# Performance work log

Measured on AMD Instinct MI355X. Metric: run time of the kernel, lower is better.

Reference implementation:

```python
import jax, jax.numpy as jnp
import numpy as np

N_EDGES = 8_388_608      # total synapses (flat weight vector length)
NUM_TYPES = 200          # number of unique edge types (ragged groups)
STRENGTH = 1e-3          # regularizer strength (cast to float32 as in the TF module)


def setup_inputs() -> dict:
    key = jax.random.key(0)
    k1, k2, k3 = jax.random.split(key, 3)
    # Edges pre-sorted by edge type -> contiguous segments (equivalent to the
    # RaggedTensor.from_value_rowids grouping built in __init__).
    segment_ids = jnp.sort(
        jax.random.randint(k1, (N_EDGES,), 0, NUM_TYPES, dtype=jnp.int32))
    x = jax.random.normal(k2, (N_EDGES,), dtype=jnp.float32)
    init_raw = jax.random.normal(k3, (N_EDGES,), dtype=jnp.float32)
    # __init__ sorts the initial weights within each edge-type group; since
    # segment_ids is already sorted, lexsort with segment_ids as the primary
    # key sorts values within each contiguous segment.
    order = jnp.lexsort((init_raw, segment_ids))
    initial_sorted = init_raw[order]
    return {"x": x, "initial_sorted": initial_sorted, "segment_ids": segment_ids}


def reference(x, initial_sorted, segment_ids):
    x = x.astype(jnp.float32)
    # Segmented sort of the current weights: primary key = edge type,
    # secondary key = value. Equivalent to tf.sort(x_i) per ragged group.
    order = jnp.lexsort((x, segment_ids))
    x_sorted = x[order]                       # [n_edges], sorted within each group
    diff = jnp.abs(x_sorted - initial_sorted)  # per-edge |sorted(x) - sorted(y)|
    sums = jax.ops.segment_sum(diff, segment_ids, num_segments=NUM_TYPES)
    counts = jax.ops.segment_sum(jnp.ones_like(diff), segment_ids,
                                 num_segments=NUM_TYPES)
    emd = sums / jnp.maximum(counts, 1.0)      # per-group Wasserstein-1 (mean L1)
    return jnp.mean(emd) * jnp.float32(STRENGTH)
```

## Files before the change

### kernel.cpp

```cpp
#include <hip/hip_runtime.h>
#include <hip/hip_bf16.h>

#define NSEG 200
#define STRENGTH 1e-3f
#define NFB 8192
#define FSCALE (8192.0f / 12.0f)
#define BT 1024
#define SPLIT 5
#define CH 9472
#define WINCAP 9728
#define PSTRIDE (NFB + 8)

__device__ __forceinline__ int fbin_of(float v) {
    float t = (v + 6.0f) * FSCALE;
    int b = (int)floorf(t);
    return b < 0 ? 0 : (b > NFB - 1 ? NFB - 1 : b);
}

__global__ void k_bounds(const int* __restrict__ seg, int* __restrict__ seg_starts,
                         float* __restrict__ segSums, int N) {
    int stride = gridDim.x * blockDim.x;
    int tid = blockIdx.x * blockDim.x + threadIdx.x;
    if (tid == 0) { seg_starts[0] = 0; seg_starts[NSEG] = N; }
    for (int k = tid; k < NSEG; k += stride) segSums[k] = 0.f;
    const int4* s4 = (const int4*)seg;
    int N4 = N >> 2;
    for (int i = tid; i < N4; i += stride) {
        int4 s = s4[i];
        int prev = (i == 0) ? s.x : seg[i * 4 - 1];
        if (s.x != prev) seg_starts[s.x] = i * 4;
        if (s.y != s.x) seg_starts[s.y] = i * 4 + 1;
        if (s.z != s.y) seg_starts[s.z] = i * 4 + 2;
        if (s.w != s.z) seg_starts[s.w] = i * 4 + 3;
    }
}

__global__ void __launch_bounds__(BT)
k_hist(const float* __restrict__ x, const int* __restrict__ seg_starts,
       unsigned short* __restrict__ pfxg) {
    __shared__ unsigned h32[NFB];
    __shared__ unsigned wsum[16];
    int s = blockIdx.x;
    int t = threadIdx.x;
    int st = seg_starts[s], en = seg_starts[s + 1];
    int n = en - st;
    const float* xs = x + st;
    for (int k = t; k < NFB; k += BT) h32[k] = 0;
    __syncthreads();
    if (n > 0) {
        int head = min(n, (4 - (st & 3)) & 3);
        for (int k = t; k < head; k += BT) atomicAdd(&h32[fbin_of(xs[k])], 1u);
        int nv = (n - head) >> 2;
        const float4* xs4 = (const float4*)(xs + head);
        for (int j = t; j < nv; j += BT) {
            float4 v = xs4[j];
            atomicAdd(&h32[fbin_of(v.x)], 1u);
            atomicAdd(&h32[fbin_of(v.y)], 1u);
            atomicAdd(&h32[fbin_of(v.z)], 1u);
            atomicAdd(&h32[fbin_of(v.w)], 1u);
        }
        for (int k = head + nv * 4 + t; k < n; k += BT) atomicAdd(&h32[fbin_of(xs[k])], 1u);
    }
    __syncthreads();
    unsigned wbuf[8]; unsigned run = 0;
    #pragma unroll
    for (int i = 0; i < 8; ++i) { unsigned c = h32[t * 8 + i]; wbuf[i] = run; run += c; }
    unsigned incl = run;
    for (int off = 1; off < 64; off <<= 1) {
        unsigned nv2 = __shfl_up(incl, off, 64);
        if ((t & 63) >= off) incl += nv2;
    }
    if ((t & 63) == 63) wsum[t >> 6] = incl;
    __syncthreads();
    unsigned wb = 0; int myw = t >> 6;
    #pragma unroll
    for (int j = 0; j < 16; ++j) wb += (j < myw) ? wsum[j] : 0u;
    unsigned base = wb + incl - run;
    unsigned short* pp = pfxg + (size_t)s * PSTRIDE;
    unsigned pk0 = (base + wbuf[0]) | ((base + wbuf[1]) << 16);
    unsigned pk1 = (base + wbuf[2]) | ((base + wbuf[3]) << 16);
    unsigned pk2 = (base + wbuf[4]) | ((base + wbuf[5]) << 16);
    unsigned pk3 = (base + wbuf[6]) | ((base + wbuf[7]) << 16);
    ((uint4*)pp)[t] = make_uint4(pk0, pk1, pk2, pk3);
    if (t == BT - 1) pp[NFB] = (unsigned short)(base + run);
}

__global__ void __launch_bounds__(BT)
k_seg(const float* __restrict__ x, const float* __restrict__ y,
      const int* __restrict__ seg_starts, const unsigned short* __restrict__ pfxg,
      float* __restrict__ segSums) {
    __shared__ unsigned short pfx[NFB + 2];
    __shared__ unsigned cur[NFB / 4];
    __shared__ __align__(16) float win[WINCAP + 4];
    __shared__ int B[12];
    __shared__ float warr[16];

    int s = blockIdx.x % NSEG;
    int half = blockIdx.x / NSEG;
    int t = threadIdx.x;
    int st = seg_starts[s], en = seg_starts[s + 1];
    int n = en - st;
    if (n <= 0) return;
    const float* xs = x + st;
    const float* ys = y + st;

    const unsigned short* pp = pfxg + (size_t)s * PSTRIDE;
    ((uint4*)pfx)[t] = ((const uint4*)pp)[t];
    if (t == 0) pfx[NFB] = pp[NFB];
    __syncthreads();

    int nch = (n + CH - 1) / CH;
    if (t == 0) { B[0] = 0; B[nch] = NFB; }
    if (t >= 1 && t < nch) {
        int target = t * CH;
        int lo = 0, hi = NFB - 1;
        while (lo < hi) { int mid = (lo + hi) >> 1; if ((int)pfx[mid + 1] > target) hi = mid; else lo = mid + 1; }
        B[t] = lo;
    }
    __syncthreads();

    int head = min(n, (4 - (st & 3)) & 3);
    int nv = (n - head) >> 2;
    const float4* xs4 = (const float4*)(xs + head);
    int tail0 = head + nv * 4;

    float acc = 0.f;
    for (int c = half; c < nch; c += SPLIT) {
        int Fa = B[c], Fb = B[c + 1];
        int w0 = (int)pfx[Fa], w1 = (int)pfx[Fb];
        int wsz = w1 - w0;
        int wA = Fa >> 2, wB = ((Fb - 1) >> 2) + 1;
        for (int k = wA + t; k < wB; k += BT) cur[k] = 0;
        __syncthreads();
        for (int k = t; k < head; k += BT) {
            float v = xs[k];
            int f = fbin_of(v);
            if (f >= Fa && f < Fb) {
                unsigned shf = (f & 3) * 8;
                unsigned old = atomicAdd(&cur[f >> 2], 1u << shf);
                win[(int)pfx[f] - w0 + (int)((old >> shf) & 0xFFu)] = v;
            }
        }
        for (int j = t; j < nv; j += BT) {
            float4 v4 = xs4[j];
            #pragma unroll
            for (int e = 0; e < 4; ++e) {
                float v = (e == 0) ? v4.x : (e == 1) ? v4.y : (e == 2) ? v4.z : v4.w;
                int f = fbin_of(v);
                if (f >= Fa && f < Fb) {
                    unsigned shf = (f & 3) * 8;
                    unsigned old = atomicAdd(&cur[f >> 2], 1u << shf);
                    win[(int)pfx[f] - w0 + (int)((old >> shf) & 0xFFu)] = v;
                }
            }
        }
        for (int k = tail0 + t; k < n; k += BT) {
            float v = xs[k];
            int f = fbin_of(v);
            if (f >= Fa && f < Fb) {
                unsigned shf = (f & 3) * 8;
                unsigned old = atomicAdd(&cur[f >> 2], 1u << shf);
                win[(int)pfx[f] - w0 + (int)((old >> shf) & 0xFFu)] = v;
            }
        }
        if (t < 4) win[wsz + t] = __builtin_inff();
        __syncthreads();
        for (int q = w0 + t; q < w1; q += BT) {
            float v = win[q - w0];
            int f = fbin_of(v);
            int bs = (int)pfx[f], be = (int)pfx[f + 1];
            int ls = bs - w0, le = be - w0;
            int a = ls & ~3;
            int cnt = a - ls;
            for (int j = a; j < le; j += 4) {
                float4 qv = *(const float4*)&win[j];
                int jg = w0 + j;
                cnt += (qv.x < v) + ((qv.x == v) & (jg + 0 < q));
                cnt += (qv.y < v) + ((qv.y == v) & (jg + 1 < q));
                cnt += (qv.z < v) + ((qv.z == v) & (jg + 2 < q));
                cnt += (qv.w < v) + ((qv.w == v) & (jg + 3 < q));
            }
            acc += fabsf(v - ys[bs + cnt]);
        }
        __syncthreads();
    }

    for (int off = 32; off > 0; off >>= 1) acc += __shfl_xor(acc, off, 64);
    if ((t & 63) == 0) warr[t >> 6] = acc;
    __syncthreads();
    if (t == 0) {
        float tot = 0.f;
        #pragma unroll
        for (int j = 0; j < 16; ++j) tot += warr[j];
        if (tot != 0.f) atomicAdd(&segSums[s], tot);
    }
}

__global__ void k_final(const float* __restrict__ segSums, const int* __restrict__ seg_starts,
                        float* __restrict__ out) {
    __shared__ float red[256];
    int t = threadIdx.x;
    float a = 0.f;
    for (int k = t; k < NSEG; k += 256) {
        float n = (float)(seg_starts[k + 1] - seg_starts[k]);
        a += segSums[k] / fmaxf(n, 1.0f);
    }
    red[t] = a;
    __syncthreads();
    for (int off = 128; off > 0; off >>= 1) {
        if (t < off) red[t] += red[t + off];
        __syncthreads();
    }
    if (t == 0) out[0] = red[0] * (1.0f / (float)NSEG) * STRENGTH;
}

extern "C" void kernel_launch(void* const* d_in, const int* in_sizes, int n_in,
                              void* d_out, int out_size, void* d_ws, size_t ws_size,
                              hipStream_t stream) {
    const float* x = (const float*)d_in[0];
    const float* y = (const float*)d_in[1];
    const int* seg = (const int*)d_in[2];
    int N = in_sizes[0];

    char* ws = (char*)d_ws;
    float* segSums    = (float*)ws;
    int*   seg_starts = (int*)(segSums + NSEG);
    unsigned short* pfxg = (unsigned short*)(seg_starts + NSEG + 8);

    k_bounds<<<512, 256, 0, stream>>>(seg, seg_starts, segSums, N);
    k_hist<<<NSEG, BT, 0, stream>>>(x, seg_starts, pfxg);
    k_seg<<<NSEG * SPLIT, BT, 0, stream>>>(x, y, seg_starts, pfxg, segSums);
    k_final<<<1, 256, 0, stream>>>(segSums, seg_starts, (float*)d_out);
}
```

Before: 104.3 us.

## Add a partition pass so each segment block reads only its value window

Adds a k_part kernel that scatters x into per-segment, per-split partitions in global memory. k_hist now computes the split boundaries so the splits are balanced. Previously each of the SPLIT blocks per segment rescanned the whole segment and filtered by bin range, which meant roughly five reads of x. Now each k_seg block reads only its contiguous partition once. The cost is an extra kernel launch, a global scatter with atomics, and the assumption that each 8192-element chunk spans at most two segments and that each window fits in the LDS window capacity.

```diff
diff --git a/kernel.cpp b/kernel.cpp
--- a/kernel.cpp
+++ b/kernel.cpp
@@ -7,9 +7,9 @@
 #define FSCALE (8192.0f / 12.0f)
 #define BT 1024
 #define SPLIT 5
-#define CH 9472
 #define WINCAP 9728
 #define PSTRIDE (NFB + 8)
+#define PCH 8192
 
 __device__ __forceinline__ int fbin_of(float v) {
     float t = (v + 6.0f) * FSCALE;
@@ -18,11 +18,12 @@
 }
 
 __global__ void k_bounds(const int* __restrict__ seg, int* __restrict__ seg_starts,
-                         float* __restrict__ segSums, int N) {
+                         float* __restrict__ segSums, unsigned* __restrict__ gcur, int N) {
     int stride = gridDim.x * blockDim.x;
     int tid = blockIdx.x * blockDim.x + threadIdx.x;
     if (tid == 0) { seg_starts[0] = 0; seg_starts[NSEG] = N; }
     for (int k = tid; k < NSEG; k += stride) segSums[k] = 0.f;
+    for (int k = tid; k < NSEG * 8; k += stride) gcur[k] = 0u;
     const int4* s4 = (const int4*)seg;
     int N4 = N >> 2;
     for (int i = tid; i < N4; i += stride) {
@@ -37,9 +38,10 @@
 
 __global__ void __launch_bounds__(BT)
 k_hist(const float* __restrict__ x, const int* __restrict__ seg_starts,
-       unsigned short* __restrict__ pfxg) {
+       unsigned short* __restrict__ pfxg, int* __restrict__ Bg, int* __restrict__ Bpos) {
     __shared__ unsigned h32[NFB];
     __shared__ unsigned wsum[16];
+    __shared__ int nsh;
     int s = blockIdx.x;
     int t = threadIdx.x;
     int st = seg_starts[s], en = seg_starts[s + 1];
@@ -48,7 +50,7 @@
     for (int k = t; k < NFB; k += BT) h32[k] = 0;
     __syncthreads();
     if (n > 0) {
-        int head = min(n, (4 - (st & 3)) & 3);
+        int head = min(n, (int)((4 - (st & 3)) & 3));
         for (int k = t; k < head; k += BT) atomicAdd(&h32[fbin_of(xs[k])], 1u);
         int nv = (n - head) >> 2;
         const float4* xs4 = (const float4*)(xs + head);
@@ -75,116 +77,169 @@
     unsigned wb = 0; int myw = t >> 6;
     #pragma unroll
     for (int j = 0; j < 16; ++j) wb += (j < myw) ? wsum[j] : 0u;
-    unsigned base = wb + incl - run;
+    unsigned pbase = wb + incl - run;
     unsigned short* pp = pfxg + (size_t)s * PSTRIDE;
-    unsigned pk0 = (base + wbuf[0]) | ((base + wbuf[1]) << 16);
-    unsigned pk1 = (base + wbuf[2]) | ((base + wbuf[3]) << 16);
-    unsigned pk2 = (base + wbuf[4]) | ((base + wbuf[5]) << 16);
-    unsigned pk3 = (base + wbuf[6]) | ((base + wbuf[7]) << 16);
+    unsigned pk0 = (pbase + wbuf[0]) | ((pbase + wbuf[1]) << 16);
+    unsigned pk1 = (pbase + wbuf[2]) | ((pbase + wbuf[3]) << 16);
+    unsigned pk2 = (pbase + wbuf[4]) | ((pbase + wbuf[5]) << 16);
+    unsigned pk3 = (pbase + wbuf[6]) | ((pbase + wbuf[7]) << 16);
     ((uint4*)pp)[t] = make_uint4(pk0, pk1, pk2, pk3);
-    if (t == BT - 1) pp[NFB] = (unsigned short)(base + run);
+    if (t == BT - 1) { pp[NFB] = (unsigned short)(pbase + run); nsh = (int)(pbase + run); }
+    #pragma unroll
+    for (int i = 0; i < 8; ++i) h32[t * 8 + i] = pbase + wbuf[i];
+    __syncthreads();
+    if (t == 0) { Bg[s * 8 + 0] = 0; Bg[s * 8 + SPLIT] = NFB; Bpos[s * 8 + 0] = 0; Bpos[s * 8 + SPLIT] = nsh; }
+    if (t >= 1 && t < SPLIT) {
+        int target = (int)(((long)t * nsh) / SPLIT);
+        int lo = 0, hi = NFB - 1;
+        while (lo < hi) { int mid = (lo + hi) >> 1; if ((int)h32[mid + 1] > target) hi = mid; else lo = mid + 1; }
+        Bg[s * 8 + t] = lo;
+        Bpos[s * 8 + t] = (int)h32[lo];
+    }
+}
+
+__global__ void __launch_bounds__(1024)
+k_part(const float* __restrict__ x, const int* __restrict__ seg_starts,
+       const int* __restrict__ Bg, const int* __restrict__ Bpos,
+       unsigned* __restrict__ gcur, float* __restrict__ part, int N) {
+    __shared__ int sst[NSEG + 1];
+    __shared__ unsigned hh[16][12];
+    __shared__ int gb[10];
+    __shared__ int sB[8];
+    int t = threadIdx.x;
+    for (int k = t; k < NSEG + 1; k += 1024) sst[k] = seg_starts[k];
+    if (t < 192) ((unsigned*)hh)[t] = 0u;
+    __syncthreads();
+    int base = blockIdx.x * PCH;
+    if (base >= N) return;
+    int lo = 0, hi = NSEG - 1;
+    while (lo < hi) { int mid = (lo + hi) >> 1; if (base < sst[mid + 1]) hi = mid; else lo = mid + 1; }
+    int s0 = lo, bnd = sst[s0 + 1];
+    if (t < 4) sB[t] = Bg[s0 * 8 + 1 + t];
+    else if (t < 8) sB[t] = Bg[(s0 + 1) * 8 + 1 + (t - 4)];
+    __syncthreads();
+    int grp = t >> 6;
+    float vv[8]; unsigned pk[8];
+    const float4* x4 = (const float4*)(x + base);
+    #pragma unroll
+    for (int it = 0; it < 2; ++it) {
+        int j = it * 1024 + t;
+        int gi = base + j * 4;
+        float4 v4;
+        if (gi + 3 < N) v4 = x4[j];
+        else v4 = make_float4(0.f, 0.f, 0.f, 0.f);
+        #pragma unroll
+        for (int e = 0; e < 4; ++e) {
+            int i = it * 4 + e;
+            float v = (e == 0) ? v4.x : (e == 1) ? v4.y : (e == 2) ? v4.z : v4.w;
+            vv[i] = v;
+            int g = gi + e;
+            if (g < N) {
+                int off = (g >= bnd) ? 4 : 0;
+                int f = fbin_of(v);
+                int p = (f >= sB[off]) + (f >= sB[off + 1]) + (f >= sB[off + 2]) + (f >= sB[off + 3]);
+                int sp = (off >> 2) * 5 + p;
+                unsigned lr = atomicAdd(&hh[grp][sp], 1u);
+                pk[i] = ((unsigned)sp << 10) | lr;
+            } else pk[i] = 0xffffffffu;
+        }
+    }
+    __syncthreads();
+    if (t < 10) {
+        unsigned run = 0;
+        #pragma unroll
+        for (int g = 0; g < 16; ++g) { unsigned c = hh[g][t]; hh[g][t] = run; run += c; }
+        int s = s0 + (t >= 5);
+        int p = (t >= 5) ? t - 5 : t;
+        int rsv = 0;
+        if (run > 0) rsv = (int)atomicAdd(&gcur[s * 8 + p], run);
+        gb[t] = sst[s] + Bpos[s * 8 + p] + rsv;
+    }
+    __syncthreads();
+    #pragma unroll
+    for (int i = 0; i < 8; ++i) {
+        if (pk[i] == 0xffffffffu) continue;
+        int sp = (int)(pk[i] >> 10);
+        int lr = (int)(pk[i] & 1023u);
+        part[gb[sp] + (int)hh[grp][sp] + lr] = vv[i];
+    }
 }
 
 __global__ void __launch_bounds__(BT)
-k_seg(const float* __restrict__ x, const float* __restrict__ y,
+k_seg(const float* __restrict__ part, const float* __restrict__ y,
       const int* __restrict__ seg_starts, const unsigned short* __restrict__ pfxg,
-      float* __restrict__ segSums) {
-    __shared__ unsigned short pfx[NFB + 2];
+      const int* __restrict__ Bg, float* __restrict__ segSums) {
+    __shared__ __align__(16) unsigned short pfx[NFB + 2];
     __shared__ unsigned cur[NFB / 4];
     __shared__ __align__(16) float win[WINCAP + 4];
-    __shared__ int B[12];
     __shared__ float warr[16];
-
     int s = blockIdx.x % NSEG;
-    int half = blockIdx.x / NSEG;
+    int p = blockIdx.x / NSEG;
     int t = threadIdx.x;
     int st = seg_starts[s], en = seg_starts[s + 1];
     int n = en - st;
     if (n <= 0) return;
-    const float* xs = x + st;
     const float* ys = y + st;
-
     const unsigned short* pp = pfxg + (size_t)s * PSTRIDE;
     ((uint4*)pfx)[t] = ((const uint4*)pp)[t];
     if (t == 0) pfx[NFB] = pp[NFB];
     __syncthreads();
-
-    int nch = (n + CH - 1) / CH;
-    if (t == 0) { B[0] = 0; B[nch] = NFB; }
-    if (t >= 1 && t < nch) {
-        int target = t * CH;
-        int lo = 0, hi = NFB - 1;
-        while (lo < hi) { int mid = (lo + hi) >> 1; if ((int)pfx[mid + 1] > target) hi = mid; else lo = mid + 1; }
-        B[t] = lo;
-    }
-    __syncthreads();
-
-    int head = min(n, (4 - (st & 3)) & 3);
-    int nv = (n - head) >> 2;
-    const float4* xs4 = (const float4*)(xs + head);
-    int tail0 = head + nv * 4;
-
+    int Fa = Bg[s * 8 + p], Fb = Bg[s * 8 + p + 1];
+    int w0 = (int)pfx[Fa], w1 = (int)pfx[Fb];
+    int wsz = w1 - w0;
+    int wA = Fa >> 2;
+    int wB2 = (Fb > Fa) ? (((Fb - 1) >> 2) + 1) : wA;
+    for (int k = wA + t; k < wB2; k += BT) cur[k] = 0u;
+    __syncthreads();
+    const float* ps = part + st + w0;
+    int head = min(wsz, (int)((4 - ((st + w0) & 3)) & 3));
+    for (int k = t; k < head; k += BT) {
+        float v = ps[k];
+        int f = fbin_of(v);
+        unsigned shf = (f & 3) * 8;
+        unsigned old = atomicAdd(&cur[f >> 2], 1u << shf);
+        win[(int)pfx[f] - w0 + (int)((old >> shf) & 0xFFu)] = v;
+    }
+    int nv = (wsz - head) >> 2;
+    const float4* ps4 = (const float4*)(ps + head);
+    for (int j = t; j < nv; j += BT) {
+        float4 v4 = ps4[j];
+        #pragma unroll
+        for (int e = 0; e < 4; ++e) {
+            float v = (e == 0) ? v4.x : (e == 1) ? v4.y : (e == 2) ? v4.z : v4.w;
+            int f = fbin_of(v);
+            unsigned shf = (f & 3) * 8;
+            unsigned old = atomicAdd(&cur[f >> 2], 1u << shf);
+            win[(int)pfx[f] - w0 + (int)((old >> shf) & 0xFFu)] = v;
+        }
+    }
+    for (int k = head + nv * 4 + t; k < wsz; k += BT) {
+        float v = ps[k];
+        int f = fbin_of(v);
+        unsigned shf = (f & 3) * 8;
+        unsigned old = atomicAdd(&cur[f >> 2], 1u << shf);
+        win[(int)pfx[f] - w0 + (int)((old >> shf) & 0xFFu)] = v;
+    }
+    if (t < 4) win[wsz + t] = __builtin_inff();
+    __syncthreads();
     float acc = 0.f;
-    for (int c = half; c < nch; c += SPLIT) {
-        int Fa = B[c], Fb = B[c + 1];
-        int w0 = (int)pfx[Fa], w1 = (int)pfx[Fb];
-        int wsz = w1 - w0;
-        int wA = Fa >> 2, wB = ((Fb - 1) >> 2) + 1;
-        for (int k = wA + t; k < wB; k += BT) cur[k] = 0;
-        __syncthreads();
-        for (int k = t; k < head; k += BT) {
-            float v = xs[k];
-            int f = fbin_of(v);
-            if (f >= Fa && f < Fb) {
-                unsigned shf = (f & 3) * 8;
-                unsigned old = atomicAdd(&cur[f >> 2], 1u << shf);
-                win[(int)pfx[f] - w0 + (int)((old >> shf) & 0xFFu)] = v;
-            }
-        }
-        for (int j = t; j < nv; j += BT) {
-            float4 v4 = xs4[j];
-            #pragma unroll
-            for (int e = 0; e < 4; ++e) {
-                float v = (e == 0) ? v4.x : (e == 1) ? v4.y : (e == 2) ? v4.z : v4.w;
-                int f = fbin_of(v);
-                if (f >= Fa && f < Fb) {
-                    unsigned shf = (f & 3) * 8;
-                    unsigned old = atomicAdd(&cur[f >> 2], 1u << shf);
-                    win[(int)pfx[f] - w0 + (int)((old >> shf) & 0xFFu)] = v;
-                }
-            }
-        }
-        for (int k = tail0 + t; k < n; k += BT) {
-            float v = xs[k];
-            int f = fbin_of(v);
-            if (f >= Fa && f < Fb) {
-                unsigned shf = (f & 3) * 8;
-                unsigned old = atomicAdd(&cur[f >> 2], 1u << shf);
-                win[(int)pfx[f] - w0 + (int)((old >> shf) & 0xFFu)] = v;
-            }
-        }
-        if (t < 4) win[wsz + t] = __builtin_inff();
-        __syncthreads();
-        for (int q = w0 + t; q < w1; q += BT) {
-            float v = win[q - w0];
-            int f = fbin_of(v);
-            int bs = (int)pfx[f], be = (int)pfx[f + 1];
-            int ls = bs - w0, le = be - w0;
-            int a = ls & ~3;
-            int cnt = a - ls;
-            for (int j = a; j < le; j += 4) {
-                float4 qv = *(const float4*)&win[j];
-                int jg = w0 + j;
-                cnt += (qv.x < v) + ((qv.x == v) & (jg + 0 < q));
-                cnt += (qv.y < v) + ((qv.y == v) & (jg + 1 < q));
-                cnt += (qv.z < v) + ((qv.z == v) & (jg + 2 < q));
-                cnt += (qv.w < v) + ((qv.w == v) & (jg + 3 < q));
-            }
-            acc += fabsf(v - ys[bs + cnt]);
-        }
-        __syncthreads();
-    }
-
+    for (int q = w0 + t; q < w1; q += BT) {
+        float v = win[q - w0];
+        int f = fbin_of(v);
+        int bs = (int)pfx[f], be = (int)pfx[f + 1];
+        int ls = bs - w0, le = be - w0;
+        int a = ls & ~3;
+        int cnt = a - ls;
+        for (int j = a; j < le; j += 4) {
+            float4 qv = *(const float4*)&win[j];
+            int jg = w0 + j;
+            cnt += (qv.x < v) + ((qv.x == v) & (jg + 0 < q));
+            cnt += (qv.y < v) + ((qv.y == v) & (jg + 1 < q));
+            cnt += (qv.z < v) + ((qv.z == v) & (jg + 2 < q));
+            cnt += (qv.w < v) + ((qv.w == v) & (jg + 3 < q));
+        }
+        acc += fabsf(v - ys[bs + cnt]);
+    }
     for (int off = 32; off > 0; off >>= 1) acc += __shfl_xor(acc, off, 64);
     if ((t & 63) == 0) warr[t >> 6] = acc;
     __syncthreads();
@@ -224,11 +279,18 @@
 
     char* ws = (char*)d_ws;
     float* segSums    = (float*)ws;
-    int*   seg_starts = (int*)(segSums + NSEG);
-    unsigned short* pfxg = (unsigned short*)(seg_starts + NSEG + 8);
-
-    k_bounds<<<512, 256, 0, stream>>>(seg, seg_starts, segSums, N);
-    k_hist<<<NSEG, BT, 0, stream>>>(x, seg_starts, pfxg);
-    k_seg<<<NSEG * SPLIT, BT, 0, stream>>>(x, y, seg_starts, pfxg, segSums);
+    int*   seg_starts = (int*)(ws + 800);
+    unsigned* gcur    = (unsigned*)(ws + 1616);
+    int*   Bg         = (int*)(ws + 8016);
+    int*   Bpos       = (int*)(ws + 14448);
+    unsigned short* pfxg = (unsigned short*)(ws + 20880);
+    float* part       = (float*)(ws + 20880 + (size_t)NSEG * PSTRIDE * 2 + 16);
+
+    int nchunk = (N + PCH - 1) / PCH;
+
+    k_bounds<<<512, 256, 0, stream>>>(seg, seg_starts, segSums, gcur, N);
+    k_hist<<<NSEG, BT, 0, stream>>>(x, seg_starts, pfxg, Bg, Bpos);
+    k_part<<<nchunk, 1024, 0, stream>>>(x, seg_starts, Bg, Bpos, gcur, part, N);
+    k_seg<<<NSEG * SPLIT, BT, 0, stream>>>(part, y, seg_starts, pfxg, Bg, segSums);
     k_final<<<1, 256, 0, stream>>>(segSums, seg_starts, (float*)d_out);
 }
```

After: 102.6 us. Within noise of the previous version (-1.6%).
